# Optimization experiments

Measured on AMD Instinct MI355X. Metric: run time of the kernel, lower is better.

Reference implementation:

```python
import jax, jax.numpy as jnp
import numpy as np

N_NODES = 100000
IN_DIM = 128
HID = 128
N_EDGES = 1600000
N_PAIRS = 500000


def setup_inputs() -> dict:
    key = jax.random.key(0)
    ks = jax.random.split(key, 16)

    def lin(k, fan_out, fan_in):
        s = 1.0 / np.sqrt(fan_in)
        kw, kb = jax.random.split(k)
        W = jax.random.uniform(kw, (fan_out, fan_in), jnp.float32, -s, s)
        b = jax.random.uniform(kb, (fan_out,), jnp.float32, -s, s)
        return W, b

    x = jax.random.normal(ks[0], (N_NODES, IN_DIM), jnp.float32)
    edge_index = jax.random.randint(ks[1], (2, N_EDGES), 0, N_NODES, jnp.int64)
    edge_pairs = jax.random.randint(ks[2], (N_PAIRS, 2), 0, N_NODES, jnp.int64)

    # SAGEConv 1: lin_l (neighbor aggr, with bias), lin_r (root, no bias)
    W1l, b1l = lin(ks[3], HID, IN_DIM)
    W1r, _ = lin(ks[4], HID, IN_DIM)
    # SAGEConv 2
    W2l, b2l = lin(ks[5], HID, HID)
    W2r, _ = lin(ks[6], HID, HID)
    # MLP decoder
    Wm1, bm1 = lin(ks[7], HID, HID)
    Wm2, bm2 = lin(ks[8], HID // 2, HID)
    Wm3, bm3 = lin(ks[9], 1, HID // 2)

    return dict(x=x, edge_index=edge_index, edge_pairs=edge_pairs,
                W1l=W1l, b1l=b1l, W1r=W1r,
                W2l=W2l, b2l=b2l, W2r=W2r,
                Wm1=Wm1, bm1=bm1, Wm2=Wm2, bm2=bm2, Wm3=Wm3, bm3=bm3)


def _sage_conv(x, src, dst, Wl, bl, Wr):
    # mean aggregation of source-node features into destination nodes
    msg_sum = jax.ops.segment_sum(x[src], dst, num_segments=N_NODES)  # [N, D]
    cnt = jax.ops.segment_sum(jnp.ones((src.shape[0],), x.dtype), dst,
                              num_segments=N_NODES)
    aggr = msg_sum / jnp.maximum(cnt, 1.0)[:, None]
    return aggr @ Wl.T + bl + x @ Wr.T


def reference(x, edge_index, edge_pairs,
              W1l, b1l, W1r, W2l, b2l, W2r,
              Wm1, bm1, Wm2, bm2, Wm3, bm3):
    src, dst = edge_index[0], edge_index[1]
    # encode (eval mode: dropout = identity)
    h = jax.nn.relu(_sage_conv(x, src, dst, W1l, b1l, W1r))
    z = _sage_conv(h, src, dst, W2l, b2l, W2r)  # [N, HID]
    # decode
    hp = z[edge_pairs[:, 0]] * z[edge_pairs[:, 1]]  # [P, HID]
    hp = jax.nn.relu(hp @ Wm1.T + bm1)
    hp = jax.nn.relu(hp @ Wm2.T + bm2)
    return (hp @ Wm3.T + bm3).squeeze(-1)  # [P]
```

## Files before the change

kernel.cpp:

```cpp
#include <hip/hip_runtime.h>
#include <stdint.h>

typedef _Float16 half8 __attribute__((ext_vector_type(8)));
typedef float float4v __attribute__((ext_vector_type(4)));

constexpr int kN = 100000;
constexpr int kE = 1600000;
constexpr int kP = 500000;
constexpr int NBS = (kN + 255) / 256;
constexpr int CT3 = kN / 16;
constexpr int DT2 = kP / 32;

__global__ void deg_slot_kernel(const int* __restrict__ dst,
                                int* __restrict__ deg, int* __restrict__ slot) {
    int e = blockIdx.x * blockDim.x + threadIdx.x;
    if (e < kE) slot[e] = atomicAdd(&deg[dst[e]], 1);
}

__global__ void scan_block_sums(const int* __restrict__ deg, int* __restrict__ bsum) {
    __shared__ int red[256];
    int t = threadIdx.x;
    int i = blockIdx.x * 256 + t;
    red[t] = (i < kN) ? deg[i] : 0;
    __syncthreads();
    for (int s = 128; s > 0; s >>= 1) {
        if (t < s) red[t] += red[t + s];
        __syncthreads();
    }
    if (t == 0) bsum[blockIdx.x] = red[0];
}

__global__ void scan_bsums(const int* __restrict__ bsum, int* __restrict__ boff) {
    __shared__ int sm[512];
    int t = threadIdx.x;
    int orig = (t < NBS) ? bsum[t] : 0;
    sm[t] = orig;
    __syncthreads();
    for (int d = 1; d < 512; d <<= 1) {
        int u = (t >= d) ? sm[t - d] : 0;
        __syncthreads();
        sm[t] += u;
        __syncthreads();
    }
    if (t < NBS) boff[t] = sm[t] - orig;
}

__global__ void scan_write(const int* __restrict__ deg, const int* __restrict__ boff,
                           int* __restrict__ row_start) {
    __shared__ int sm[256];
    int t = threadIdx.x;
    int i = blockIdx.x * 256 + t;
    int v = (i < kN) ? deg[i] : 0;
    sm[t] = v;
    __syncthreads();
    for (int d = 1; d < 256; d <<= 1) {
        int u = (t >= d) ? sm[t - d] : 0;
        __syncthreads();
        sm[t] += u;
        __syncthreads();
    }
    int excl = sm[t] - v + boff[blockIdx.x];
    if (i < kN) row_start[i] = excl;
    if (i == kN - 1) row_start[kN] = excl + v;
}

__global__ void fill2_kernel(const int* __restrict__ src, const int* __restrict__ dst,
                             const int* __restrict__ row_start,
                             const int* __restrict__ slot, int* __restrict__ srcs) {
    int e = blockIdx.x * blockDim.x + threadIdx.x;
    if (e < kE) srcs[row_start[dst[e]] + slot[e]] = src[e];
}

__global__ void cvt_x_kernel(const float* __restrict__ x, _Float16* __restrict__ xh) {
    const int i = (blockIdx.x * 256 + threadIdx.x) * 8;
    if (i >= kN * 128) return;
    const float4 a = *(const float4*)&x[i];
    const float4 b = *(const float4*)&x[i + 4];
    half8 v;
    v[0] = (_Float16)a.x; v[1] = (_Float16)a.y; v[2] = (_Float16)a.z; v[3] = (_Float16)a.w;
    v[4] = (_Float16)b.x; v[5] = (_Float16)b.y; v[6] = (_Float16)b.z; v[7] = (_Float16)b.w;
    *(half8*)&xh[i] = v;
}

__global__ void cvt_w_kernel(
    const float* __restrict__ W1l, const float* __restrict__ W1r,
    const float* __restrict__ W2l, const float* __restrict__ W2r,
    const float* __restrict__ Wm1, const float* __restrict__ Wm2,
    _Float16* __restrict__ CW1h, _Float16* __restrict__ CW1e,
    _Float16* __restrict__ CW2h, _Float16* __restrict__ CW2e,
    _Float16* __restrict__ M1h,  _Float16* __restrict__ M2h)
{
    const int i = blockIdx.x * 256 + threadIdx.x;
    if (i < 32768) {
        const int o = i >> 8, k = i & 255;
        const float w = (k < 128) ? W1l[o * 128 + k] : W1r[o * 128 + k - 128];
        const _Float16 h = (_Float16)w;
        CW1h[i] = h; CW1e[i] = (_Float16)(w - (float)h);
    } else if (i < 65536) {
        const int j = i - 32768;
        const int o = j >> 8, k = j & 255;
        const float w = (k < 128) ? W2l[o * 128 + k] : W2r[o * 128 + k - 128];
        const _Float16 h = (_Float16)w;
        CW2h[j] = h; CW2e[j] = (_Float16)(w - (float)h);
    } else if (i < 81920) {
        const int j = i - 65536;
        M1h[j] = (_Float16)Wm1[j];
    } else if (i < 90112) {
        const int j = i - 81920;
        M2h[j] = (_Float16)Wm2[j];
    }
}

template <bool RELU>
__global__ __launch_bounds__(256, 4) void conv_mfma(
    const _Float16* __restrict__ xin,
    const int* __restrict__ row_start,
    const int* __restrict__ srcs,
    const _Float16* __restrict__ Wh,
    const _Float16* __restrict__ We,
    const float* __restrict__ bias,
    _Float16* __restrict__ out)
{
    __shared__ __align__(16) _Float16 stg_all[4 * 16 * 136];
    const int wInB = threadIdx.x >> 6;
    _Float16* stg  = &stg_all[wInB * (16 * 136)];
    const int l = threadIdx.x & 63;
    const int p = l & 15;
    const int q = l >> 4;
    const int tile = blockIdx.x * 4 + wInB;
    if (tile >= CT3) return;
    const int c = p * 8;
    const int lbase = l & 48;

    int j0[4], j1[4];
#pragma unroll
    for (int s = 0; s < 4; s++) {
        const int n = tile * 16 + s * 4 + q;
        j0[s] = row_start[n];
        j1[s] = row_start[n + 1];
    }
    int idx16[4];
#pragma unroll
    for (int s = 0; s < 4; s++) {
        const int tA = j0[s] + p;
        const int v  = srcs[tA];
        idx16[s] = (tA < j1[s]) ? v : 0;
    }

    for (int s = 0; s < 4; s++) {
        const int cnt = j1[s] - j0[s];
        float facc[8];
#pragma unroll
        for (int u = 0; u < 8; u++) facc[u] = 0.f;
        int h = 0;
        for (int jc = j0[s]; jc < j1[s]; jc += 8, h++) {
            int myidx;
            if (h < 2) {
                myidx = idx16[s];
            } else {
                const int tB = jc + (p & 7);
                const int v  = srcs[tB];
                myidx = (tB < j1[s]) ? v : 0;
            }
            const int lsh = lbase + ((h == 1) ? 8 : 0);
            half8 rows[8];
#pragma unroll
            for (int i = 0; i < 8; i++) {
                const int sidx = __shfl(myidx, lsh + i);
                rows[i] = *(const half8*)&xin[(size_t)sidx * 128 + c];
            }
            const int rem = j1[s] - jc;
#pragma unroll
            for (int i = 0; i < 8; i++) {
                if (i < rem) {
#pragma unroll
                    for (int u = 0; u < 8; u++) facc[u] += (float)rows[i][u];
                }
            }
        }
        const float inv = 1.0f / (float)(cnt > 1 ? cnt : 1);
        half8 hv;
#pragma unroll
        for (int u = 0; u < 8; u++) hv[u] = (_Float16)(facc[u] * inv);
        *(half8*)&stg[(s * 4 + q) * 136 + c] = hv;
    }

    half8 rt[4];
#pragma unroll
    for (int kt = 0; kt < 4; kt++)
        rt[kt] = *(const half8*)&xin[(size_t)(tile * 16 + p) * 128 + kt * 32 + q * 8];

    half8 am[4];
#pragma unroll
    for (int kt = 0; kt < 4; kt++)
        am[kt] = *(const half8*)&stg[p * 136 + kt * 32 + q * 8];

    float4v acc[8];
#pragma unroll
    for (int nt = 0; nt < 8; nt++) {
        const float b = bias[nt * 16 + p];
        acc[nt][0] = b; acc[nt][1] = b; acc[nt][2] = b; acc[nt][3] = b;
    }
#pragma unroll
    for (int kt = 0; kt < 8; kt++) {
        const half8 a = (kt < 4) ? am[kt] : rt[kt - 4];
#pragma unroll
        for (int nt = 0; nt < 8; nt++) {
            const int widx = (nt * 16 + p) * 256 + kt * 32 + q * 8;
            const half8 bh = *(const half8*)&Wh[widx];
            const half8 be = *(const half8*)&We[widx];
            acc[nt] = __builtin_amdgcn_mfma_f32_16x16x32_f16(a, bh, acc[nt], 0, 0, 0);
            acc[nt] = __builtin_amdgcn_mfma_f32_16x16x32_f16(a, be, acc[nt], 0, 0, 0);
        }
    }

#pragma unroll
    for (int nt = 0; nt < 8; nt++)
#pragma unroll
        for (int r = 0; r < 4; r++) {
            float v = acc[nt][r];
            if (RELU) v = fmaxf(v, 0.f);
            stg[(q * 4 + r) * 136 + nt * 16 + p] = (_Float16)v;
        }
    {
        const int row = l >> 2;
        const int c2  = (l & 3) * 8;
#pragma unroll
        for (int i = 0; i < 4; i++)
            *(half8*)&out[(size_t)(tile * 16 + row) * 128 + i * 32 + c2] =
                *(const half8*)&stg[row * 136 + i * 32 + c2];
    }
}

__global__ __launch_bounds__(256, 3) void decoder_mfma(
    const _Float16* __restrict__ z,
    const int* __restrict__ pairs,
    const _Float16* __restrict__ M1h, const float* __restrict__ bm1,
    const _Float16* __restrict__ M2h, const float* __restrict__ bm2,
    const float* __restrict__ Wm3, const float* __restrict__ bm3,
    float* __restrict__ outv)
{
    __shared__ __align__(16) _Float16 buf_all[4 * 32 * 136];
    const int wInB = threadIdx.x >> 6;
    _Float16* buf  = &buf_all[wInB * (32 * 136)];
    const int l = threadIdx.x & 63;
    const int p = l & 15;
    const int q = l >> 4;
    const int tile = blockIdx.x * 4 + wInB;
    if (tile >= DT2) return;
    const int c = p * 8;

    int2 ab[8];
#pragma unroll
    for (int it = 0; it < 8; it++)
        ab[it] = *(const int2*)&pairs[(size_t)(tile * 32 + it * 4 + q) * 2];
    half8 za[8], zb[8];
#pragma unroll
    for (int it = 0; it < 8; it++) {
        za[it] = *(const half8*)&z[(size_t)ab[it].x * 128 + c];
        zb[it] = *(const half8*)&z[(size_t)ab[it].y * 128 + c];
    }
#pragma unroll
    for (int it = 0; it < 8; it++)
        *(half8*)&buf[(it * 4 + q) * 136 + c] = za[it] * zb[it];

    half8 a1[2][4];
#pragma unroll
    for (int m = 0; m < 2; m++)
#pragma unroll
        for (int kt = 0; kt < 4; kt++)
            a1[m][kt] = *(const half8*)&buf[(m * 16 + p) * 136 + kt * 32 + q * 8];

    float4v acc1[2][8];
#pragma unroll
    for (int nt = 0; nt < 8; nt++) {
        const float b = bm1[nt * 16 + p];
#pragma unroll
        for (int m = 0; m < 2; m++) {
            acc1[m][nt][0] = b; acc1[m][nt][1] = b; acc1[m][nt][2] = b; acc1[m][nt][3] = b;
        }
    }
#pragma unroll
    for (int kt = 0; kt < 4; kt++)
#pragma unroll
        for (int nt = 0; nt < 8; nt++) {
            const half8 bh = *(const half8*)&M1h[(nt * 16 + p) * 128 + kt * 32 + q * 8];
            acc1[0][nt] = __builtin_amdgcn_mfma_f32_16x16x32_f16(a1[0][kt], bh, acc1[0][nt], 0, 0, 0);
            acc1[1][nt] = __builtin_amdgcn_mfma_f32_16x16x32_f16(a1[1][kt], bh, acc1[1][nt], 0, 0, 0);
        }

#pragma unroll
    for (int m = 0; m < 2; m++)
#pragma unroll
        for (int nt = 0; nt < 8; nt++)
#pragma unroll
            for (int r = 0; r < 4; r++)
                buf[(m * 16 + q * 4 + r) * 136 + nt * 16 + p] =
                    (_Float16)fmaxf(acc1[m][nt][r], 0.f);

    half8 a2[2][4];
#pragma unroll
    for (int m = 0; m < 2; m++)
#pragma unroll
        for (int kt = 0; kt < 4; kt++)
            a2[m][kt] = *(const half8*)&buf[(m * 16 + p) * 136 + kt * 32 + q * 8];

    float4v acc2[2][4];
#pragma unroll
    for (int nt = 0; nt < 4; nt++) {
        const float b = bm2[nt * 16 + p];
#pragma unroll
        for (int m = 0; m < 2; m++) {
            acc2[m][nt][0] = b; acc2[m][nt][1] = b; acc2[m][nt][2] = b; acc2[m][nt][3] = b;
        }
    }
#pragma unroll
    for (int kt = 0; kt < 4; kt++)
#pragma unroll
        for (int nt = 0; nt < 4; nt++) {
            const half8 bh = *(const half8*)&M2h[(nt * 16 + p) * 128 + kt * 32 + q * 8];
            acc2[0][nt] = __builtin_amdgcn_mfma_f32_16x16x32_f16(a2[0][kt], bh, acc2[0][nt], 0, 0, 0);
            acc2[1][nt] = __builtin_amdgcn_mfma_f32_16x16x32_f16(a2[1][kt], bh, acc2[1][nt], 0, 0, 0);
        }

    float wm3v[4];
#pragma unroll
    for (int nt = 0; nt < 4; nt++) wm3v[nt] = Wm3[nt * 16 + p];
    const float b3 = bm3[0];
#pragma unroll
    for (int m = 0; m < 2; m++) {
        float part[4];
#pragma unroll
        for (int r = 0; r < 4; r++) part[r] = 0.f;
#pragma unroll
        for (int nt = 0; nt < 4; nt++)
#pragma unroll
            for (int r = 0; r < 4; r++)
                part[r] += fmaxf(acc2[m][nt][r], 0.f) * wm3v[nt];
#pragma unroll
        for (int s = 1; s <= 8; s <<= 1)
#pragma unroll
            for (int r = 0; r < 4; r++) part[r] += __shfl_xor(part[r], s);
        if (p == 0) {
            float4 o = make_float4(part[0] + b3, part[1] + b3, part[2] + b3, part[3] + b3);
            *(float4*)&outv[tile * 32 + m * 16 + q * 4] = o;
        }
    }
}

extern "C" void kernel_launch(void* const* d_in, const int* in_sizes, int n_in,
                              void* d_out, int out_size, void* d_ws, size_t ws_size,
                              hipStream_t stream) {
    const float* x   = (const float*)d_in[0];
    const int*   src = (const int*)d_in[1];
    const int*   dst = src + kE;
    const int*   ep  = (const int*)d_in[2];
    const float* W1l = (const float*)d_in[3];
    const float* b1l = (const float*)d_in[4];
    const float* W1r = (const float*)d_in[5];
    const float* W2l = (const float*)d_in[6];
    const float* b2l = (const float*)d_in[7];
    const float* W2r = (const float*)d_in[8];
    const float* Wm1 = (const float*)d_in[9];
    const float* bm1 = (const float*)d_in[10];
    const float* Wm2 = (const float*)d_in[11];
    const float* bm2 = (const float*)d_in[12];
    const float* Wm3 = (const float*)d_in[13];
    const float* bm3 = (const float*)d_in[14];
    float* outv = (float*)d_out;

    char* ws = (char*)d_ws;
    size_t off = 0;
    auto alloc = [&](size_t bytes) -> void* {
        void* p = ws + off;
        off += bytes;
        off = (off + 255) & ~(size_t)255;
        return p;
    };
    int*      deg       = (int*)alloc((size_t)kN * 4);
    int*      row_start = (int*)alloc((size_t)(kN + 1) * 4);
    int*      slot      = (int*)alloc((size_t)kE * 4);
    int*      bsum      = (int*)alloc(512 * 4);
    int*      boff      = (int*)alloc(512 * 4);
    int*      srcs      = (int*)alloc((size_t)(kE + 64) * 4);
    _Float16* xh        = (_Float16*)alloc((size_t)kN * 128 * 2);
    _Float16* hh        = (_Float16*)alloc((size_t)kN * 128 * 2);
    _Float16* zh        = (_Float16*)alloc((size_t)kN * 128 * 2);
    _Float16* CW1h      = (_Float16*)alloc(128 * 256 * 2);
    _Float16* CW1e      = (_Float16*)alloc(128 * 256 * 2);
    _Float16* CW2h      = (_Float16*)alloc(128 * 256 * 2);
    _Float16* CW2e      = (_Float16*)alloc(128 * 256 * 2);
    _Float16* M1h       = (_Float16*)alloc(128 * 128 * 2);
    _Float16* M2h       = (_Float16*)alloc(64 * 128 * 2);

    hipMemsetAsync(deg, 0, (size_t)kN * sizeof(int), stream);
    deg_slot_kernel<<<(kE + 255) / 256, 256, 0, stream>>>(dst, deg, slot);
    scan_block_sums<<<NBS, 256, 0, stream>>>(deg, bsum);
    scan_bsums<<<1, 512, 0, stream>>>(bsum, boff);
    scan_write<<<NBS, 256, 0, stream>>>(deg, boff, row_start);
    fill2_kernel<<<(kE + 255) / 256, 256, 0, stream>>>(src, dst, row_start, slot, srcs);

    cvt_x_kernel<<<(kN * 128 / 8 + 255) / 256, 256, 0, stream>>>(x, xh);
    cvt_w_kernel<<<352, 256, 0, stream>>>(W1l, W1r, W2l, W2r, Wm1, Wm2,
                                          CW1h, CW1e, CW2h, CW2e, M1h, M2h);

    const int convBlocks = (CT3 + 3) / 4;
    conv_mfma<true><<<convBlocks, 256, 0, stream>>>(xh, row_start, srcs, CW1h, CW1e, b1l, hh);
    conv_mfma<false><<<convBlocks, 256, 0, stream>>>(hh, row_start, srcs, CW2h, CW2e, b2l, zh);

    const int decBlocks = (DT2 + 3) / 4;
    decoder_mfma<<<decBlocks, 256, 0, stream>>>(
        zh, ep, M1h, bm1, M2h, bm2, Wm3, bm3, outv);
}
```

Measured before the change: 615.7 us.

## Double-buffer neighbor gathers in conv and split decoder into two prefetched passes

The conv aggregation loop becomes one flat loop over all four destination rows. The next 8-row gather is issued into a second register buffer before the current one is accumulated, so gather latency overlaps with the FP adds. The decoder now processes two 16-pair tiles one after the other, prefetching the second tile's z rows while the first tile's MFMAs run, which halves the LDS footprint and the accumulator registers. This adds more control flow and extra live registers for the prefetch buffers, and zero-degree rows now need an explicit zero-fill.

```diff
diff --git a/kernel.cpp b/kernel.cpp
--- a/kernel.cpp
+++ b/kernel.cpp
@@ -9,7 +9,7 @@
 constexpr int kP = 500000;
 constexpr int NBS = (kN + 255) / 256;
 constexpr int CT3 = kN / 16;
-constexpr int DT2 = kP / 32;
+constexpr int DT3 = kP / 16;
 
 __global__ void deg_slot_kernel(const int* __restrict__ dst,
                                 int* __restrict__ deg, int* __restrict__ slot) {
@@ -147,43 +147,77 @@
         idx16[s] = (tA < j1[s]) ? v : 0;
     }
 
-    for (int s = 0; s < 4; s++) {
-        const int cnt = j1[s] - j0[s];
-        float facc[8];
-#pragma unroll
-        for (int u = 0; u < 8; u++) facc[u] = 0.f;
-        int h = 0;
-        for (int jc = j0[s]; jc < j1[s]; jc += 8, h++) {
-            int myidx;
-            if (h < 2) {
-                myidx = idx16[s];
-            } else {
-                const int tB = jc + (p & 7);
-                const int v  = srcs[tB];
-                myidx = (tB < j1[s]) ? v : 0;
+    half8 buf0[8], buf1[8];
+
+    auto issueE = [&](int s, int jc, half8* B) {
+        const int off = jc - j0[s];
+        int myidx;
+        if (off < 16) {
+            myidx = idx16[s];
+        } else {
+            const int tB = jc + (p & 7);
+            const int v  = srcs[tB];
+            myidx = (tB < j1[s]) ? v : 0;
+        }
+        const int lsh = lbase + ((off == 8) ? 8 : 0);
+#pragma unroll
+        for (int i = 0; i < 8; i++) {
+            const int sidx = __shfl(myidx, lsh + i);
+            B[i] = *(const half8*)&xin[(size_t)sidx * 128 + c];
+        }
+    };
+    auto adv = [&](int& s, int& jc) {
+        jc += 8;
+        if (jc >= j1[s]) {
+            s++;
+            while (s < 4 && j0[s] >= j1[s]) s++;
+            jc = (s < 4) ? j0[s] : 0;
+        }
+    };
+
+    int s_cur = 0;
+    while (s_cur < 4 && j0[s_cur] >= j1[s_cur]) s_cur++;
+    int jc_cur = (s_cur < 4) ? j0[s_cur] : 0;
+    if (s_cur < 4) issueE(s_cur, jc_cur, buf0);
+
+    float facc[8];
+    int par = 0;
+    while (s_cur < 4) {
+        int s_nxt = s_cur, jc_nxt = jc_cur;
+        adv(s_nxt, jc_nxt);
+        if (s_nxt < 4) issueE(s_nxt, jc_nxt, par ? buf0 : buf1);
+
+        half8* B = par ? buf1 : buf0;
+        if (jc_cur == j0[s_cur]) {
+#pragma unroll
+            for (int u = 0; u < 8; u++) facc[u] = 0.f;
+        }
+        const int rem = j1[s_cur] - jc_cur;
+#pragma unroll
+        for (int i = 0; i < 8; i++) {
+            if (i < rem) {
+#pragma unroll
+                for (int u = 0; u < 8; u++) facc[u] += (float)B[i][u];
             }
-            const int lsh = lbase + ((h == 1) ? 8 : 0);
-            half8 rows[8];
-#pragma unroll
-            for (int i = 0; i < 8; i++) {
-                const int sidx = __shfl(myidx, lsh + i);
-                rows[i] = *(const half8*)&xin[(size_t)sidx * 128 + c];
-            }
-            const int rem = j1[s] - jc;
-#pragma unroll
-            for (int i = 0; i < 8; i++) {
-                if (i < rem) {
-#pragma unroll
-                    for (int u = 0; u < 8; u++) facc[u] += (float)rows[i][u];
-                }
-            }
-        }
-        const float inv = 1.0f / (float)(cnt > 1 ? cnt : 1);
-        half8 hv;
-#pragma unroll
-        for (int u = 0; u < 8; u++) hv[u] = (_Float16)(facc[u] * inv);
-        *(half8*)&stg[(s * 4 + q) * 136 + c] = hv;
-    }
+        }
+        if (rem <= 8) {
+            const int cnt = j1[s_cur] - j0[s_cur];
+            const float inv = 1.0f / (float)(cnt > 1 ? cnt : 1);
+            half8 hv;
+#pragma unroll
+            for (int u = 0; u < 8; u++) hv[u] = (_Float16)(facc[u] * inv);
+            *(half8*)&stg[(s_cur * 4 + q) * 136 + c] = hv;
+        }
+        s_cur = s_nxt; jc_cur = jc_nxt; par ^= 1;
+    }
+#pragma unroll
+    for (int s = 0; s < 4; s++)
+        if (j0[s] >= j1[s]) {
+            half8 zv;
+#pragma unroll
+            for (int u = 0; u < 8; u++) zv[u] = (_Float16)0.f;
+            *(half8*)&stg[(s * 4 + q) * 136 + c] = zv;
+        }
 
     half8 rt[4];
 #pragma unroll
@@ -240,95 +274,106 @@
     const float* __restrict__ Wm3, const float* __restrict__ bm3,
     float* __restrict__ outv)
 {
-    __shared__ __align__(16) _Float16 buf_all[4 * 32 * 136];
+    __shared__ __align__(16) _Float16 buf_all[4 * 16 * 136];
     const int wInB = threadIdx.x >> 6;
-    _Float16* buf  = &buf_all[wInB * (32 * 136)];
+    _Float16* buf  = &buf_all[wInB * (16 * 136)];
     const int l = threadIdx.x & 63;
     const int p = l & 15;
     const int q = l >> 4;
-    const int tile = blockIdx.x * 4 + wInB;
-    if (tile >= DT2) return;
+    const int wid = blockIdx.x * 4 + wInB;
+    const int tA = wid * 2;
+    if (tA >= DT3) return;
+    const int tB = tA + 1;
     const int c = p * 8;
 
-    int2 ab[8];
-#pragma unroll
-    for (int it = 0; it < 8; it++)
-        ab[it] = *(const int2*)&pairs[(size_t)(tile * 32 + it * 4 + q) * 2];
-    half8 za[8], zb[8];
-#pragma unroll
-    for (int it = 0; it < 8; it++) {
-        za[it] = *(const half8*)&z[(size_t)ab[it].x * 128 + c];
-        zb[it] = *(const half8*)&z[(size_t)ab[it].y * 128 + c];
-    }
-#pragma unroll
-    for (int it = 0; it < 8; it++)
-        *(half8*)&buf[(it * 4 + q) * 136 + c] = za[it] * zb[it];
-
-    half8 a1[2][4];
-#pragma unroll
-    for (int m = 0; m < 2; m++)
+    const float b3 = bm3[0];
+    float wm3v[4], bm1v[8], bm2v[4];
+#pragma unroll
+    for (int nt = 0; nt < 4; nt++) wm3v[nt] = Wm3[nt * 16 + p];
+#pragma unroll
+    for (int nt = 0; nt < 8; nt++) bm1v[nt] = bm1[nt * 16 + p];
+#pragma unroll
+    for (int nt = 0; nt < 4; nt++) bm2v[nt] = bm2[nt * 16 + p];
+
+    int2 abA[4], abB[4];
+#pragma unroll
+    for (int it = 0; it < 4; it++) {
+        abA[it] = *(const int2*)&pairs[(size_t)(tA * 16 + it * 4 + q) * 2];
+        abB[it] = *(const int2*)&pairs[(size_t)(tB * 16 + it * 4 + q) * 2];
+    }
+
+    half8 za[4], zb[4];
+#pragma unroll
+    for (int it = 0; it < 4; it++) {
+        za[it] = *(const half8*)&z[(size_t)abA[it].x * 128 + c];
+        zb[it] = *(const half8*)&z[(size_t)abA[it].y * 128 + c];
+    }
+
+    half8 zaB[4], zbB[4];
+
+#pragma unroll
+    for (int pass = 0; pass < 2; pass++) {
+        const int t = (pass == 0) ? tA : tB;
+
+#pragma unroll
+        for (int it = 0; it < 4; it++) {
+            const half8 pa = (pass == 0) ? za[it] : zaB[it];
+            const half8 pb = (pass == 0) ? zb[it] : zbB[it];
+            *(half8*)&buf[(it * 4 + q) * 136 + c] = pa * pb;
+        }
+
+        half8 a1[4];
 #pragma unroll
         for (int kt = 0; kt < 4; kt++)
-            a1[m][kt] = *(const half8*)&buf[(m * 16 + p) * 136 + kt * 32 + q * 8];
-
-    float4v acc1[2][8];
-#pragma unroll
-    for (int nt = 0; nt < 8; nt++) {
-        const float b = bm1[nt * 16 + p];
-#pragma unroll
-        for (int m = 0; m < 2; m++) {
-            acc1[m][nt][0] = b; acc1[m][nt][1] = b; acc1[m][nt][2] = b; acc1[m][nt][3] = b;
-        }
-    }
-#pragma unroll
-    for (int kt = 0; kt < 4; kt++)
+            a1[kt] = *(const half8*)&buf[p * 136 + kt * 32 + q * 8];
+
+        if (pass == 0) {
+#pragma unroll
+            for (int it = 0; it < 4; it++) {
+                zaB[it] = *(const half8*)&z[(size_t)abB[it].x * 128 + c];
+                zbB[it] = *(const half8*)&z[(size_t)abB[it].y * 128 + c];
+            }
+        }
+
+        float4v acc1[8];
 #pragma unroll
         for (int nt = 0; nt < 8; nt++) {
-            const half8 bh = *(const half8*)&M1h[(nt * 16 + p) * 128 + kt * 32 + q * 8];
-            acc1[0][nt] = __builtin_amdgcn_mfma_f32_16x16x32_f16(a1[0][kt], bh, acc1[0][nt], 0, 0, 0);
-            acc1[1][nt] = __builtin_amdgcn_mfma_f32_16x16x32_f16(a1[1][kt], bh, acc1[1][nt], 0, 0, 0);
-        }
-
-#pragma unroll
-    for (int m = 0; m < 2; m++)
+            const float b = bm1v[nt];
+            acc1[nt][0] = b; acc1[nt][1] = b; acc1[nt][2] = b; acc1[nt][3] = b;
+        }
+#pragma unroll
+        for (int kt = 0; kt < 4; kt++)
+#pragma unroll
+            for (int nt = 0; nt < 8; nt++) {
+                const half8 bh = *(const half8*)&M1h[(nt * 16 + p) * 128 + kt * 32 + q * 8];
+                acc1[nt] = __builtin_amdgcn_mfma_f32_16x16x32_f16(a1[kt], bh, acc1[nt], 0, 0, 0);
+            }
+
 #pragma unroll
         for (int nt = 0; nt < 8; nt++)
 #pragma unroll
             for (int r = 0; r < 4; r++)
-                buf[(m * 16 + q * 4 + r) * 136 + nt * 16 + p] =
-                    (_Float16)fmaxf(acc1[m][nt][r], 0.f);
-
-    half8 a2[2][4];
-#pragma unroll
-    for (int m = 0; m < 2; m++)
+                buf[(q * 4 + r) * 136 + nt * 16 + p] = (_Float16)fmaxf(acc1[nt][r], 0.f);
+
+        half8 a2[4];
 #pragma unroll
         for (int kt = 0; kt < 4; kt++)
-            a2[m][kt] = *(const half8*)&buf[(m * 16 + p) * 136 + kt * 32 + q * 8];
-
-    float4v acc2[2][4];
-#pragma unroll
-    for (int nt = 0; nt < 4; nt++) {
-        const float b = bm2[nt * 16 + p];
-#pragma unroll
-        for (int m = 0; m < 2; m++) {
-            acc2[m][nt][0] = b; acc2[m][nt][1] = b; acc2[m][nt][2] = b; acc2[m][nt][3] = b;
-        }
-    }
-#pragma unroll
-    for (int kt = 0; kt < 4; kt++)
+            a2[kt] = *(const half8*)&buf[p * 136 + kt * 32 + q * 8];
+
+        float4v acc2[4];
 #pragma unroll
         for (int nt = 0; nt < 4; nt++) {
-            const half8 bh = *(const half8*)&M2h[(nt * 16 + p) * 128 + kt * 32 + q * 8];
-            acc2[0][nt] = __builtin_amdgcn_mfma_f32_16x16x32_f16(a2[0][kt], bh, acc2[0][nt], 0, 0, 0);
-            acc2[1][nt] = __builtin_amdgcn_mfma_f32_16x16x32_f16(a2[1][kt], bh, acc2[1][nt], 0, 0, 0);
-        }
-
-    float wm3v[4];
-#pragma unroll
-    for (int nt = 0; nt < 4; nt++) wm3v[nt] = Wm3[nt * 16 + p];
-    const float b3 = bm3[0];
-#pragma unroll
-    for (int m = 0; m < 2; m++) {
+            const float b = bm2v[nt];
+            acc2[nt][0] = b; acc2[nt][1] = b; acc2[nt][2] = b; acc2[nt][3] = b;
+        }
+#pragma unroll
+        for (int kt = 0; kt < 4; kt++)
+#pragma unroll
+            for (int nt = 0; nt < 4; nt++) {
+                const half8 bh = *(const half8*)&M2h[(nt * 16 + p) * 128 + kt * 32 + q * 8];
+                acc2[nt] = __builtin_amdgcn_mfma_f32_16x16x32_f16(a2[kt], bh, acc2[nt], 0, 0, 0);
+            }
+
         float part[4];
 #pragma unroll
         for (int r = 0; r < 4; r++) part[r] = 0.f;
@@ -336,14 +381,14 @@
         for (int nt = 0; nt < 4; nt++)
 #pragma unroll
             for (int r = 0; r < 4; r++)
-                part[r] += fmaxf(acc2[m][nt][r], 0.f) * wm3v[nt];
+                part[r] += fmaxf(acc2[nt][r], 0.f) * wm3v[nt];
 #pragma unroll
         for (int s = 1; s <= 8; s <<= 1)
 #pragma unroll
             for (int r = 0; r < 4; r++) part[r] += __shfl_xor(part[r], s);
         if (p == 0) {
             float4 o = make_float4(part[0] + b3, part[1] + b3, part[2] + b3, part[3] + b3);
-            *(float4*)&outv[tile * 32 + m * 16 + q * 4] = o;
+            *(float4*)&outv[t * 16 + q * 4] = o;
         }
     }
 }
@@ -408,7 +453,7 @@
     conv_mfma<true><<<convBlocks, 256, 0, stream>>>(xh, row_start, srcs, CW1h, CW1e, b1l, hh);
     conv_mfma<false><<<convBlocks, 256, 0, stream>>>(hh, row_start, srcs, CW2h, CW2e, b2l, zh);
 
-    const int decBlocks = (DT2 + 3) / 4;
+    const int decBlocks = (DT3 / 2 + 3) / 4;
     decoder_mfma<<<decBlocks, 256, 0, stream>>>(
         zh, ep, M1h, bm1, M2h, bm2, Wm3, bm3, outv);
 }
```

Result: slower. 829.3 us (+34.7%).
